# Optimization experiments

Hardware: AMD Instinct MI355X
Metric: run time of the kernel (lower is better)

The kernel has to match this reference:

```python
import jax, jax.numpy as jnp
import numpy as np

B, S, D = 4, 2048, 1024
E = 16          # num_experts
K = 2           # num_experts_per_tok
F = 512         # moe_intermediate_size
FS = 2048       # shared_expert_intermediate_size


def setup_inputs() -> dict:
    key = jax.random.key(0)
    ks = jax.random.split(key, 9)
    s = 0.02
    return {
        "hidden_states": jax.random.normal(ks[0], (B, S, D), jnp.float32),
        "router_w": jax.random.normal(ks[1], (E, D), jnp.float32) * s,   # torch Linear-style [out,in]
        "Wg": jax.random.normal(ks[2], (E, D, F), jnp.float32) * s,      # gate_proj per expert
        "Wu": jax.random.normal(ks[3], (E, D, F), jnp.float32) * s,      # up_proj per expert
        "Wd": jax.random.normal(ks[4], (E, F, D), jnp.float32) * s,      # down_proj per expert
        "Sg": jax.random.normal(ks[5], (D, FS), jnp.float32) * s,        # shared expert gate_proj
        "Su": jax.random.normal(ks[6], (D, FS), jnp.float32) * s,        # shared expert up_proj
        "Sd": jax.random.normal(ks[7], (FS, D), jnp.float32) * s,        # shared expert down_proj
        "shared_gate_w": jax.random.normal(ks[8], (D, 1), jnp.float32) * s,
    }


def reference(hidden_states, router_w, Wg, Wu, Wd, Sg, Su, Sd, shared_gate_w):
    b, s, d = hidden_states.shape
    x = hidden_states.reshape(-1, d)                      # [T, D]
    T = x.shape[0]

    # --- router (Qwen3NextTopKRouter): fp32 softmax -> topk -> renorm ---
    logits = jnp.einsum("td,ed->te", x.astype(jnp.float32), router_w.astype(jnp.float32))
    probs = jax.nn.softmax(logits, axis=-1)               # [T, E]
    top_w, top_i = jax.lax.top_k(probs, K)                # [T, K]
    top_w = top_w / jnp.sum(top_w, axis=-1, keepdims=True)  # norm_topk_prob
    top_w = top_w.astype(x.dtype)

    # dense combine weights [T, E]: zero except at selected experts (index_add semantics)
    dense_w = jnp.zeros((T, E), x.dtype).at[jnp.arange(T)[:, None], top_i].add(top_w)

    # --- experts: SwiGLU per expert, scan over the fixed expert axis ---
    def body(acc, params):
        wg, wu, wd, cw = params                            # cw: [T]
        h = jax.nn.silu(x @ wg) * (x @ wu)                 # [T, F]
        return acc + cw[:, None] * (h @ wd), None

    expert_out, _ = jax.lax.scan(body, jnp.zeros_like(x), (Wg, Wu, Wd, dense_w.T))

    # --- shared expert with sigmoid gate ---
    shared = (jax.nn.silu(x @ Sg) * (x @ Su)) @ Sd         # [T, D]
    shared = jax.nn.sigmoid(x @ shared_gate_w) * shared

    out = expert_out + shared
    return out.reshape(b, s, d)
```

## Files before the change

### kernel.cpp

```cpp
#include <hip/hip_runtime.h>

typedef __attribute__((ext_vector_type(8))) short short8;
typedef __attribute__((ext_vector_type(4))) float f32x4;
typedef unsigned short u16;
typedef unsigned int u32;

#define DEVI __device__ __forceinline__

DEVI u16 f2b(float f) {
  u32 u = __float_as_uint(f);
  u32 r = u + 0x7FFFu + ((u >> 16) & 1u);
  return (u16)(r >> 16);
}
DEVI float b2f(u16 h) { return __uint_as_float(((u32)h) << 16); }
DEVI float silu(float g) { return g / (1.f + __expf(-g)); }

constexpr int T_ = 8192, D_ = 1024, E_ = 16, F_ = 512, FS_ = 2048;

constexpr size_t OFF_XB   = 0;
constexpr size_t OFF_WGU  = OFF_XB  + (size_t)T_ * D_ * 2;
constexpr size_t OFF_WDT  = OFF_WGU + (size_t)E_ * 2 * F_ * D_ * 2;
constexpr size_t OFF_SGU  = OFF_WDT + (size_t)E_ * D_ * F_ * 2;
constexpr size_t OFF_SDT  = OFF_SGU + (size_t)2 * FS_ * D_ * 2;
constexpr size_t OFF_HB   = OFF_SDT + (size_t)D_ * FS_ * 2;
constexpr size_t OFF_HS   = OFF_HB  + (size_t)2 * T_ * F_ * 2;
constexpr size_t OFF_PAIR = OFF_HS  + (size_t)T_ * FS_ * 2;
constexpr size_t OFF_PW   = OFF_PAIR + (size_t)2 * T_ * D_ * 2;
constexpr size_t OFF_GATE = OFF_PW  + (size_t)2 * T_ * 4;
constexpr size_t OFF_CNT  = OFF_GATE + (size_t)T_ * 4;
constexpr size_t OFF_TOP2 = OFF_CNT + 64;
constexpr size_t OFF_LIST = OFF_TOP2 + (size_t)T_ * 4;

__global__ void prep_kernel(
    const float4* __restrict__ x4, const float4* __restrict__ rw4,
    const float4* __restrict__ sgw4, int* __restrict__ top2e,
    float* __restrict__ pw, float* __restrict__ gate, ushort4* __restrict__ xb4,
    const float* __restrict__ Wg, const float* __restrict__ Wu, const float* __restrict__ Wd,
    const float* __restrict__ Sg, const float* __restrict__ Su, const float* __restrict__ Sd,
    u16* __restrict__ wgu, u16* __restrict__ wdT,
    u16* __restrict__ sgu, u16* __restrict__ sdT) {
  const int tid = threadIdx.x;
  const int bid = blockIdx.x;
  if (bid >= 7680) {
    const int lane = tid & 63, wid = tid >> 6;
    const int t = (bid - 7680) * 4 + wid;
    const float4* xr = x4 + (size_t)t * (D_ / 4);
    float acc[17];
#pragma unroll
    for (int e = 0; e < 17; ++e) acc[e] = 0.f;
    ushort4 xo[4];
#pragma unroll
    for (int j = 0; j < 4; ++j) {
      const int d4 = j * 64 + lane;
      float4 xv = xr[d4];
      xo[j] = make_ushort4(f2b(xv.x), f2b(xv.y), f2b(xv.z), f2b(xv.w));
#pragma unroll
      for (int e = 0; e < 16; ++e) {
        float4 wv = rw4[e * 256 + d4];
        acc[e] = fmaf(xv.x, wv.x, fmaf(xv.y, wv.y, fmaf(xv.z, wv.z, fmaf(xv.w, wv.w, acc[e]))));
      }
      float4 sv = sgw4[d4];
      acc[16] = fmaf(xv.x, sv.x, fmaf(xv.y, sv.y, fmaf(xv.z, sv.z, fmaf(xv.w, sv.w, acc[16]))));
    }
#pragma unroll
    for (int j = 0; j < 4; ++j)
      xb4[(size_t)t * 256 + j * 64 + lane] = xo[j];
#pragma unroll
    for (int e = 0; e < 17; ++e) {
      float v = acc[e];
#pragma unroll
      for (int off = 32; off; off >>= 1) v += __shfl_xor(v, off);
      acc[e] = v;
    }
    if (lane == 0) {
      int i1 = 0; float l1 = acc[0];
#pragma unroll
      for (int e = 1; e < 16; ++e) if (acc[e] > l1) { l1 = acc[e]; i1 = e; }
      int i2 = (i1 == 0) ? 1 : 0; float l2 = acc[i2];
#pragma unroll
      for (int e = 0; e < 16; ++e) {
        if (e == i1) continue;
        if (acc[e] > l2) { l2 = acc[e]; i2 = e; }
      }
      float w1 = 1.f / (1.f + expf(l2 - l1));
      top2e[t] = i1 | (i2 << 8);
      pw[2 * t] = w1;
      pw[2 * t + 1] = 1.f - w1;
      gate[t] = 1.f / (1.f + expf(-acc[16]));
    }
    return;
  }
  __shared__ float lds[64][65];
  int i = bid;
  const float* in; u16* out; int R, C, mode, rem;
  if (i < 6144) {
    int j = i >> 11; rem = i & 2047;
    int b = rem >> 7; rem &= 127;
    if (j == 0)      { in = Wg + (size_t)b * D_ * F_; out = wgu + (size_t)b * 2 * F_ * D_; R = D_; C = F_;  mode = 0; }
    else if (j == 1) { in = Wu + (size_t)b * D_ * F_; out = wgu + (size_t)b * 2 * F_ * D_; R = D_; C = F_;  mode = 1; }
    else             { in = Wd + (size_t)b * F_ * D_; out = wdT + (size_t)b * D_ * F_;     R = F_; C = D_;  mode = 2; }
  } else {
    int r2 = i - 6144; int j = r2 >> 9; rem = r2 & 511;
    if (j == 0)      { in = Sg; out = sgu; R = D_;  C = FS_; mode = 0; }
    else if (j == 1) { in = Su; out = sgu; R = D_;  C = FS_; mode = 1; }
    else             { in = Sd; out = sdT; R = FS_; C = D_;  mode = 2; }
  }
  const int ntx = C >> 6;
  const int cx = rem % ntx, cy = rem / ntx;
  const int c0 = cx * 64, r0 = cy * 64;
  {
    const int tx4 = (tid & 15) * 4, ty = tid >> 4;
#pragma unroll
    for (int p = 0; p < 4; ++p) {
      const int rr = ty + p * 16;
      float4 v = *(const float4*)&in[(size_t)(r0 + rr) * C + c0 + tx4];
      lds[rr][tx4] = v.x; lds[rr][tx4 + 1] = v.y; lds[rr][tx4 + 2] = v.z; lds[rr][tx4 + 3] = v.w;
    }
  }
  __syncthreads();
  {
    const int ol = tid >> 2, seg = tid & 3;
    const int f = c0 + ol;
    size_t orow;
    if (mode == 2) orow = f;
    else orow = (size_t)((f >> 4) << 5) + (f & 15) + (mode == 1 ? 16 : 0);
    u16 vals[16];
#pragma unroll
    for (int k = 0; k < 16; ++k) vals[k] = f2b(lds[seg * 16 + k][ol]);
    u16* dst = out + orow * R + r0 + seg * 16;
    *(short8*)dst = *(short8*)&vals[0];
    *(short8*)(dst + 8) = *(short8*)&vals[8];
  }
}

__global__ __launch_bounds__(256) void compact_kernel(
    const int* __restrict__ top2e, int* __restrict__ lists, int* __restrict__ counts) {
  const int e = blockIdx.x;
  const int tid = threadIdx.x, lane = tid & 63, wid = tid >> 6;
  __shared__ int wsum[4];
  __shared__ int base;
  if (tid == 0) base = 0;
  __syncthreads();
  for (int c0 = 0; c0 < T_; c0 += 256) {
    const int t = c0 + tid;
    const int pk = top2e[t];
    int slot = -1;
    if ((pk & 0xFF) == e) slot = 2 * t;
    else if (((pk >> 8) & 0xFF) == e) slot = 2 * t + 1;
    const unsigned long long m = __ballot(slot >= 0);
    const int myofs = __popcll(m & ((1ULL << lane) - 1ULL));
    if (lane == 0) wsum[wid] = __popcll(m);
    __syncthreads();
    const int b = base;
    int wbase = 0;
#pragma unroll
    for (int w = 0; w < 4; ++w) if (w < wid) wbase += wsum[w];
    if (slot >= 0) lists[e * T_ + b + wbase + myofs] = slot;
    __syncthreads();
    if (tid == 0) base += wsum[0] + wsum[1] + wsum[2] + wsum[3];
    __syncthreads();
  }
  if (tid == 0) counts[e] = base;
}

DEVI void gl_lds16(const void* gsrc, void* lds) {
  __builtin_amdgcn_global_load_lds((const __attribute__((address_space(1))) unsigned int*)gsrc,
                                   (__attribute__((address_space(3))) unsigned int*)lds, 16, 0, 0);
}

DEVI void prefix16(const int* counts, int e, int& cnt, int& roff) {
  cnt = counts[e];
  int s = 0;
#pragma unroll
  for (int k = 0; k < E_; ++k) s += (k < e) ? counts[k] : 0;
  roff = s;
}

__global__ __launch_bounds__(256, 2) void gu_gemm(
    const u16* __restrict__ xb, const u16* __restrict__ wgu, const u16* __restrict__ sgu,
    u16* __restrict__ hb, u16* __restrict__ hs,
    const int* __restrict__ counts, const int* __restrict__ lists) {
  extern __shared__ char smem[];
  const int tid = threadIdx.x;
  const int bid = blockIdx.x;
  const bool se = (bid >= 2048);
  int mt, nt, e = 0, cnt = 0, roff = 0;
  const u16* B0;
  if (!se) {
    e = bid >> 7; int r = bid & 127; mt = r >> 3; nt = r & 7;
    prefix16(counts, e, cnt, roff);
    if (mt * 128 >= cnt) return;
    B0 = wgu + (size_t)e * 2 * F_ * D_;
  } else {
    int st = bid - 2048;
    mt = st & 63; nt = st >> 6;
    B0 = sgu;
  }

  const int lane = tid & 63, wid = tid >> 6;
  const int wm = wid >> 1, wn = wid & 1;
  const int lr = lane & 15, lg = lane >> 4;
  const int ldsrow = tid >> 3;
  const int kslot = (tid & 7) << 4;
  constexpr size_t strideB = (size_t)D_ * 2;
  const char* aSrc[4]; const char* bSrc[4];
#pragma unroll
  for (int q = 0; q < 4; ++q) {
    int row = q * 32 + ldsrow;
    int kb = kslot ^ ((row & 7) << 4);
    int r = mt * 128 + row;
    long arow;
    if (!se) arow = (r < cnt) ? (lists[e * T_ + r] >> 1) : 0;
    else arow = r;
    aSrc[q] = (const char*)xb + (size_t)arow * strideB + kb;
    int nrow = nt * 128 + row;
    bSrc[q] = (const char*)B0 + (size_t)nrow * strideB + kb;
  }

  const f32x4 fz = {0.f, 0.f, 0.f, 0.f};
  f32x4 acc[4][4];
#pragma unroll
  for (int i = 0; i < 4; ++i)
#pragma unroll
    for (int j = 0; j < 4; ++j) acc[i][j] = fz;

  const int sw = (lr & 7) << 4;
  constexpr int nks = D_ / 64;

  {
    char* dst = smem;
#pragma unroll
    for (int q = 0; q < 4; ++q) gl_lds16(aSrc[q], dst + q * 4096 + tid * 16);
#pragma unroll
    for (int q = 0; q < 4; ++q) gl_lds16(bSrc[q], dst + 16384 + q * 4096 + tid * 16);
  }
  __syncthreads();

  int cur = 0;
  for (int ks = 0; ks < nks; ++ks) {
    if (ks + 1 < nks) {
      const int kbo = (ks + 1) * 128;
      char* dst = smem + (cur ^ 1) * 32768;
#pragma unroll
      for (int q = 0; q < 4; ++q) gl_lds16(aSrc[q] + kbo, dst + q * 4096 + tid * 16);
#pragma unroll
      for (int q = 0; q < 4; ++q) gl_lds16(bSrc[q] + kbo, dst + 16384 + q * 4096 + tid * 16);
    }
    const char* As = smem + cur * 32768;
    const char* Bs = As + 16384;
#pragma unroll
    for (int kk = 0; kk < 2; ++kk) {
      const int ko = kk * 64 + lg * 16;
      short8 af[4];
#pragma unroll
      for (int fm = 0; fm < 4; ++fm) {
        int row = wm * 64 + fm * 16 + lr;
        af[fm] = *(const short8*)(As + row * 128 + (ko ^ sw));
      }
#pragma unroll
      for (int fn = 0; fn < 4; ++fn) {
        int col = wn * 64 + fn * 16 + lr;
        short8 bf = *(const short8*)(Bs + col * 128 + (ko ^ sw));
#pragma unroll
        for (int fm = 0; fm < 4; ++fm)
          acc[fm][fn] = __builtin_amdgcn_mfma_f32_16x16x32_bf16(af[fm], bf, acc[fm][fn], 0, 0, 0);
      }
    }
    __syncthreads();
    cur ^= 1;
  }

  const int c0 = 16 * (4 * nt + 2 * wn);
  const int r0 = mt * 128;
#pragma unroll
  for (int fm = 0; fm < 4; ++fm) {
#pragma unroll
    for (int j = 0; j < 4; ++j) {
      const int r = r0 + wm * 64 + fm * 16 + lg * 4 + j;
      if (!se && r >= cnt) continue;
      float h0 = silu(acc[fm][0][j]) * acc[fm][1][j];
      float h1 = silu(acc[fm][2][j]) * acc[fm][3][j];
      if (!se) {
        hb[(size_t)(roff + r) * F_ + c0 + lr] = f2b(h0);
        hb[(size_t)(roff + r) * F_ + c0 + 16 + lr] = f2b(h1);
      } else {
        hs[(size_t)r * FS_ + c0 + lr] = f2b(h0);
        hs[(size_t)r * FS_ + c0 + 16 + lr] = f2b(h1);
      }
    }
  }
}

template <int MODE>
__global__ __launch_bounds__(256, 2) void moe_gemm(
    const u16* __restrict__ Abase, const u16* __restrict__ B0,
    u16* __restrict__ outb, float* __restrict__ outf,
    const int* __restrict__ counts, const int* __restrict__ lists,
    const float* __restrict__ pw, const float* __restrict__ gate,
    const u16* __restrict__ pairb, int Kdim) {
  extern __shared__ char smem[];
  const int tid = threadIdx.x;
  const int mt = blockIdx.x, nt = blockIdx.y, e = blockIdx.z;

  int cnt = 0;
  const u16* A = Abase;
  if constexpr (MODE == 1) {
    int roff;
    prefix16(counts, e, cnt, roff);
    if (mt * 128 >= cnt) return;
    A = Abase + (size_t)roff * Kdim;
    B0 += (size_t)e * D_ * F_;
  }

  const int lane = tid & 63, wid = tid >> 6;
  const int wm = wid >> 1, wn = wid & 1;
  const int lr = lane & 15, lg = lane >> 4;
  const int ldsrow = tid >> 3;
  const int kslot = (tid & 7) << 4;
  const size_t strideB = (size_t)Kdim * 2;
  const char* aSrc[4]; const char* bSrc[4];
#pragma unroll
  for (int q = 0; q < 4; ++q) {
    int row = q * 32 + ldsrow;
    int kb = kslot ^ ((row & 7) << 4);
    long arow;
    if constexpr (MODE == 1) {
      int r = mt * 128 + row;
      arow = (r < cnt) ? r : (cnt - 1);
    } else {
      arow = mt * 128 + row;
    }
    aSrc[q] = (const char*)A + (size_t)arow * strideB + kb;
    int nrow = nt * 128 + row;
    bSrc[q] = (const char*)B0 + (size_t)nrow * strideB + kb;
  }

  const f32x4 fz = {0.f, 0.f, 0.f, 0.f};
  f32x4 acc[4][4];
#pragma unroll
  for (int i = 0; i < 4; ++i)
#pragma unroll
    for (int j = 0; j < 4; ++j) acc[i][j] = fz;

  const int nks = Kdim >> 6;
  const int sw = (lr & 7) << 4;

  {
    char* dst = smem;
#pragma unroll
    for (int q = 0; q < 4; ++q) gl_lds16(aSrc[q], dst + q * 4096 + tid * 16);
#pragma unroll
    for (int q = 0; q < 4; ++q) gl_lds16(bSrc[q], dst + 16384 + q * 4096 + tid * 16);
  }
  __syncthreads();

  int cur = 0;
  for (int ks = 0; ks < nks; ++ks) {
    if (ks + 1 < nks) {
      const int kbo = (ks + 1) * 128;
      char* dst = smem + (cur ^ 1) * 32768;
#pragma unroll
      for (int q = 0; q < 4; ++q) gl_lds16(aSrc[q] + kbo, dst + q * 4096 + tid * 16);
#pragma unroll
      for (int q = 0; q < 4; ++q) gl_lds16(bSrc[q] + kbo, dst + 16384 + q * 4096 + tid * 16);
    }
    const char* As = smem + cur * 32768;
    const char* Bs = As + 16384;
#pragma unroll
    for (int kk = 0; kk < 2; ++kk) {
      const int ko = kk * 64 + lg * 16;
      short8 af[4];
#pragma unroll
      for (int fm = 0; fm < 4; ++fm) {
        int row = wm * 64 + fm * 16 + lr;
        af[fm] = *(const short8*)(As + row * 128 + (ko ^ sw));
      }
#pragma unroll
      for (int fn = 0; fn < 4; ++fn) {
        int col = wn * 64 + fn * 16 + lr;
        short8 bf = *(const short8*)(Bs + col * 128 + (ko ^ sw));
#pragma unroll
        for (int fm = 0; fm < 4; ++fm)
          acc[fm][fn] = __builtin_amdgcn_mfma_f32_16x16x32_bf16(af[fm], bf, acc[fm][fn], 0, 0, 0);
      }
    }
    __syncthreads();
    cur ^= 1;
  }

  const int r0 = mt * 128;
#pragma unroll
  for (int fm = 0; fm < 4; ++fm) {
#pragma unroll
    for (int j = 0; j < 4; ++j) {
      const int rowt = wm * 64 + fm * 16 + lg * 4 + j;
      const int r = r0 + rowt;
      if constexpr (MODE == 1) {
        if (r >= cnt) continue;
      }
      int slot = 0;
      float rsc = 0.f;
      if constexpr (MODE == 1) { slot = lists[e * T_ + r]; rsc = pw[slot]; }
      if constexpr (MODE == 3) rsc = gate[r];
#pragma unroll
      for (int fn = 0; fn < 4; ++fn) {
        const int c = nt * 128 + wn * 64 + fn * 16 + lr;
        float v = acc[fm][fn][j];
        if constexpr (MODE == 1) {
          outb[(size_t)slot * D_ + c] = f2b(rsc * v);
        } else {
          float o = v * rsc + b2f(pairb[(size_t)(2 * r) * D_ + c]) + b2f(pairb[(size_t)(2 * r + 1) * D_ + c]);
          outf[(size_t)r * D_ + c] = o;
        }
      }
    }
  }
}

extern "C" void kernel_launch(void* const* d_in, const int* in_sizes, int n_in,
                              void* d_out, int out_size, void* d_ws, size_t ws_size,
                              hipStream_t stream) {
  const float* x   = (const float*)d_in[0];
  const float* rw  = (const float*)d_in[1];
  const float* Wg  = (const float*)d_in[2];
  const float* Wu  = (const float*)d_in[3];
  const float* Wd  = (const float*)d_in[4];
  const float* Sg  = (const float*)d_in[5];
  const float* Su  = (const float*)d_in[6];
  const float* Sd  = (const float*)d_in[7];
  const float* sgw = (const float*)d_in[8];
  float* out = (float*)d_out;

  unsigned char* ws = (unsigned char*)d_ws;
  u16* xb    = (u16*)(ws + OFF_XB);
  u16* wgu   = (u16*)(ws + OFF_WGU);
  u16* wdT   = (u16*)(ws + OFF_WDT);
  u16* sgu   = (u16*)(ws + OFF_SGU);
  u16* sdT   = (u16*)(ws + OFF_SDT);
  u16* hb    = (u16*)(ws + OFF_HB);
  u16* hs    = (u16*)(ws + OFF_HS);
  u16* pairb = (u16*)(ws + OFF_PAIR);
  float* pwf   = (float*)(ws + OFF_PW);
  float* gatef = (float*)(ws + OFF_GATE);
  int* cnti    = (int*)(ws + OFF_CNT);
  int* top2i   = (int*)(ws + OFF_TOP2);
  int* listsi  = (int*)(ws + OFF_LIST);

  prep_kernel<<<9728, 256, 0, stream>>>(
      (const float4*)x, (const float4*)rw, (const float4*)sgw,
      top2i, pwf, gatef, (ushort4*)xb,
      Wg, Wu, Wd, Sg, Su, Sd, wgu, wdT, sgu, sdT);
  compact_kernel<<<E_, 256, 0, stream>>>(top2i, listsi, cnti);

  gu_gemm<<<4096, 256, 65536, stream>>>(xb, wgu, sgu, hb, hs, cnti, listsi);
  moe_gemm<1><<<dim3(16, 8, 16), 256, 65536, stream>>>(hb, wdT, pairb, nullptr,
                                                       cnti, listsi, pwf, gatef, nullptr, 512);
  moe_gemm<3><<<dim3(64, 8, 1), 256, 65536, stream>>>(hs, sdT, nullptr, out,
                                                      cnti, listsi, pwf, gatef, pairb, 2048);

  (void)in_sizes; (void)n_in; (void)out_size; (void)ws_size;
}
```

Baseline: 302.6 us.

## Split K-step into half-stages with fine-grained vmcnt waits and new LDS layout

```diff
diff --git a/kernel.cpp b/kernel.cpp
--- a/kernel.cpp
+++ b/kernel.cpp
@@ -14,6 +14,10 @@
 }
 DEVI float b2f(u16 h) { return __uint_as_float(((u32)h) << 16); }
 DEVI float silu(float g) { return g / (1.f + __expf(-g)); }
+
+DEVI void vm8() { asm volatile("s_waitcnt vmcnt(8)" ::: "memory"); }
+DEVI void vm4() { asm volatile("s_waitcnt vmcnt(4)" ::: "memory"); }
+DEVI void vm0() { asm volatile("s_waitcnt vmcnt(0)" ::: "memory"); }
 
 constexpr int T_ = 8192, D_ = 1024, E_ = 16, F_ = 512, FS_ = 2048;
 
@@ -176,6 +180,52 @@
   roff = s;
 }
 
+#define COMPUTE_KK(base, kk)                                                      \
+  {                                                                               \
+    const char* As_ = (base);                                                     \
+    const char* Bs_ = (base) + 16384;                                             \
+    short8 af[4];                                                                 \
+    _Pragma("unroll")                                                             \
+    for (int fm = 0; fm < 4; ++fm)                                                \
+      af[fm] = *(const short8*)(As_ + (kk) * 8192 + (wm * 64 + fm * 16 + lr) * 64 + rsw); \
+    _Pragma("unroll")                                                             \
+    for (int fn = 0; fn < 4; ++fn) {                                              \
+      short8 bf = *(const short8*)(Bs_ + (kk) * 8192 + (wn * 64 + fn * 16 + lr) * 64 + rsw); \
+      _Pragma("unroll")                                                           \
+      for (int fm = 0; fm < 4; ++fm)                                              \
+        acc[fm][fn] = __builtin_amdgcn_mfma_f32_16x16x32_bf16(af[fm], bf, acc[fm][fn], 0, 0, 0); \
+    }                                                                             \
+  }
+
+#define STAGE_H0(d, o)                                        \
+  { gl_lds16(aR0 + (o), (d) + tid * 16);                      \
+    gl_lds16(aR1 + (o), (d) + 4096 + tid * 16);               \
+    gl_lds16(bR0 + (o), (d) + 16384 + tid * 16);              \
+    gl_lds16(bR1 + (o), (d) + 16384 + 4096 + tid * 16); }
+#define STAGE_H1(d, o)                                        \
+  { gl_lds16(aR0 + (o) + 64, (d) + 8192 + tid * 16);          \
+    gl_lds16(aR1 + (o) + 64, (d) + 8192 + 4096 + tid * 16);   \
+    gl_lds16(bR0 + (o) + 64, (d) + 24576 + tid * 16);         \
+    gl_lds16(bR1 + (o) + 64, (d) + 24576 + 4096 + tid * 16); }
+
+#define KLOOP(NKS)                                            \
+  STAGE_H0(smem, 0); STAGE_H1(smem, 0);                       \
+  int c_ = 0;                                                 \
+  for (int ks = 0; ks < (NKS); ++ks) {                        \
+    const bool pre = (ks + 1 < (NKS));                        \
+    const int o = (ks + 1) * 128;                             \
+    char* d = smem + (c_ ^ 1) * 32768;                        \
+    if (pre) STAGE_H0(d, o);                                  \
+    if (pre) vm8(); else vm4();                               \
+    __builtin_amdgcn_s_barrier();                             \
+    COMPUTE_KK(smem + c_ * 32768, 0);                         \
+    if (pre) STAGE_H1(d, o);                                  \
+    if (pre) vm8(); else vm0();                               \
+    __builtin_amdgcn_s_barrier();                             \
+    COMPUTE_KK(smem + c_ * 32768, 1);                         \
+    c_ ^= 1;                                                  \
+  }
+
 __global__ __launch_bounds__(256, 2) void gu_gemm(
     const u16* __restrict__ xb, const u16* __restrict__ wgu, const u16* __restrict__ sgu,
     u16* __restrict__ hb, u16* __restrict__ hs,
@@ -200,22 +250,23 @@
   const int lane = tid & 63, wid = tid >> 6;
   const int wm = wid >> 1, wn = wid & 1;
   const int lr = lane & 15, lg = lane >> 4;
-  const int ldsrow = tid >> 3;
-  const int kslot = (tid & 7) << 4;
+  const int rsw = (lg ^ ((lr >> 1) & 3)) << 4;
+
+  const int sq = tid >> 2;
+  const int scol = ((tid & 3) ^ ((tid >> 3) & 3)) << 4;
   constexpr size_t strideB = (size_t)D_ * 2;
-  const char* aSrc[4]; const char* bSrc[4];
-#pragma unroll
-  for (int q = 0; q < 4; ++q) {
-    int row = q * 32 + ldsrow;
-    int kb = kslot ^ ((row & 7) << 4);
-    int r = mt * 128 + row;
-    long arow;
-    if (!se) arow = (r < cnt) ? (lists[e * T_ + r] >> 1) : 0;
-    else arow = r;
-    aSrc[q] = (const char*)xb + (size_t)arow * strideB + kb;
-    int nrow = nt * 128 + row;
-    bSrc[q] = (const char*)B0 + (size_t)nrow * strideB + kb;
-  }
+  long ar0, ar1;
+  if (!se) {
+    int r0i = mt * 128 + sq, r1i = mt * 128 + 64 + sq;
+    ar0 = (r0i < cnt) ? (lists[e * T_ + r0i] >> 1) : 0;
+    ar1 = (r1i < cnt) ? (lists[e * T_ + r1i] >> 1) : 0;
+  } else {
+    ar0 = mt * 128 + sq; ar1 = mt * 128 + 64 + sq;
+  }
+  const char* aR0 = (const char*)xb + (size_t)ar0 * strideB + scol;
+  const char* aR1 = (const char*)xb + (size_t)ar1 * strideB + scol;
+  const char* bR0 = (const char*)B0 + (size_t)(nt * 128 + sq) * strideB + scol;
+  const char* bR1 = (const char*)B0 + (size_t)(nt * 128 + 64 + sq) * strideB + scol;
 
   const f32x4 fz = {0.f, 0.f, 0.f, 0.f};
   f32x4 acc[4][4];
@@ -224,51 +275,7 @@
 #pragma unroll
     for (int j = 0; j < 4; ++j) acc[i][j] = fz;
 
-  const int sw = (lr & 7) << 4;
-  constexpr int nks = D_ / 64;
-
-  {
-    char* dst = smem;
-#pragma unroll
-    for (int q = 0; q < 4; ++q) gl_lds16(aSrc[q], dst + q * 4096 + tid * 16);
-#pragma unroll
-    for (int q = 0; q < 4; ++q) gl_lds16(bSrc[q], dst + 16384 + q * 4096 + tid * 16);
-  }
-  __syncthreads();
-
-  int cur = 0;
-  for (int ks = 0; ks < nks; ++ks) {
-    if (ks + 1 < nks) {
-      const int kbo = (ks + 1) * 128;
-      char* dst = smem + (cur ^ 1) * 32768;
-#pragma unroll
-      for (int q = 0; q < 4; ++q) gl_lds16(aSrc[q] + kbo, dst + q * 4096 + tid * 16);
-#pragma unroll
-      for (int q = 0; q < 4; ++q) gl_lds16(bSrc[q] + kbo, dst + 16384 + q * 4096 + tid * 16);
-    }
-    const char* As = smem + cur * 32768;
-    const char* Bs = As + 16384;
-#pragma unroll
-    for (int kk = 0; kk < 2; ++kk) {
-      const int ko = kk * 64 + lg * 16;
-      short8 af[4];
-#pragma unroll
-      for (int fm = 0; fm < 4; ++fm) {
-        int row = wm * 64 + fm * 16 + lr;
-        af[fm] = *(const short8*)(As + row * 128 + (ko ^ sw));
-      }
-#pragma unroll
-      for (int fn = 0; fn < 4; ++fn) {
-        int col = wn * 64 + fn * 16 + lr;
-        short8 bf = *(const short8*)(Bs + col * 128 + (ko ^ sw));
-#pragma unroll
-        for (int fm = 0; fm < 4; ++fm)
-          acc[fm][fn] = __builtin_amdgcn_mfma_f32_16x16x32_bf16(af[fm], bf, acc[fm][fn], 0, 0, 0);
-      }
-    }
-    __syncthreads();
-    cur ^= 1;
-  }
+  KLOOP(16);
 
   const int c0 = 16 * (4 * nt + 2 * wn);
   const int r0 = mt * 128;
@@ -315,25 +322,23 @@
   const int lane = tid & 63, wid = tid >> 6;
   const int wm = wid >> 1, wn = wid & 1;
   const int lr = lane & 15, lg = lane >> 4;
-  const int ldsrow = tid >> 3;
-  const int kslot = (tid & 7) << 4;
+  const int rsw = (lg ^ ((lr >> 1) & 3)) << 4;
+
+  const int sq = tid >> 2;
+  const int scol = ((tid & 3) ^ ((tid >> 3) & 3)) << 4;
   const size_t strideB = (size_t)Kdim * 2;
-  const char* aSrc[4]; const char* bSrc[4];
-#pragma unroll
-  for (int q = 0; q < 4; ++q) {
-    int row = q * 32 + ldsrow;
-    int kb = kslot ^ ((row & 7) << 4);
-    long arow;
-    if constexpr (MODE == 1) {
-      int r = mt * 128 + row;
-      arow = (r < cnt) ? r : (cnt - 1);
-    } else {
-      arow = mt * 128 + row;
-    }
-    aSrc[q] = (const char*)A + (size_t)arow * strideB + kb;
-    int nrow = nt * 128 + row;
-    bSrc[q] = (const char*)B0 + (size_t)nrow * strideB + kb;
-  }
+  long ar0, ar1;
+  if constexpr (MODE == 1) {
+    int r0i = mt * 128 + sq, r1i = mt * 128 + 64 + sq;
+    ar0 = (r0i < cnt) ? r0i : (cnt - 1);
+    ar1 = (r1i < cnt) ? r1i : (cnt - 1);
+  } else {
+    ar0 = mt * 128 + sq; ar1 = mt * 128 + 64 + sq;
+  }
+  const char* aR0 = (const char*)A + (size_t)ar0 * strideB + scol;
+  const char* aR1 = (const char*)A + (size_t)ar1 * strideB + scol;
+  const char* bR0 = (const char*)B0 + (size_t)(nt * 128 + sq) * strideB + scol;
+  const char* bR1 = (const char*)B0 + (size_t)(nt * 128 + 64 + sq) * strideB + scol;
 
   const f32x4 fz = {0.f, 0.f, 0.f, 0.f};
   f32x4 acc[4][4];
@@ -343,50 +348,7 @@
     for (int j = 0; j < 4; ++j) acc[i][j] = fz;
 
   const int nks = Kdim >> 6;
-  const int sw = (lr & 7) << 4;
-
-  {
-    char* dst = smem;
-#pragma unroll
-    for (int q = 0; q < 4; ++q) gl_lds16(aSrc[q], dst + q * 4096 + tid * 16);
-#pragma unroll
-    for (int q = 0; q < 4; ++q) gl_lds16(bSrc[q], dst + 16384 + q * 4096 + tid * 16);
-  }
-  __syncthreads();
-
-  int cur = 0;
-  for (int ks = 0; ks < nks; ++ks) {
-    if (ks + 1 < nks) {
-      const int kbo = (ks + 1) * 128;
-      char* dst = smem + (cur ^ 1) * 32768;
-#pragma unroll
-      for (int q = 0; q < 4; ++q) gl_lds16(aSrc[q] + kbo, dst + q * 4096 + tid * 16);
-#pragma unroll
-      for (int q = 0; q < 4; ++q) gl_lds16(bSrc[q] + kbo, dst + 16384 + q * 4096 + tid * 16);
-    }
-    const char* As = smem + cur * 32768;
-    const char* Bs = As + 16384;
-#pragma unroll
-    for (int kk = 0; kk < 2; ++kk) {
-      const int ko = kk * 64 + lg * 16;
-      short8 af[4];
-#pragma unroll
-      for (int fm = 0; fm < 4; ++fm) {
-        int row = wm * 64 + fm * 16 + lr;
-        af[fm] = *(const short8*)(As + row * 128 + (ko ^ sw));
-      }
-#pragma unroll
-      for (int fn = 0; fn < 4; ++fn) {
-        int col = wn * 64 + fn * 16 + lr;
-        short8 bf = *(const short8*)(Bs + col * 128 + (ko ^ sw));
-#pragma unroll
-        for (int fm = 0; fm < 4; ++fm)
-          acc[fm][fn] = __builtin_amdgcn_mfma_f32_16x16x32_bf16(af[fm], bf, acc[fm][fn], 0, 0, 0);
-      }
-    }
-    __syncthreads();
-    cur ^= 1;
-  }
+  KLOOP(nks);
 
   const int r0 = mt * 128;
 #pragma unroll
```

Result: slower. 317.6 us (+4.9%).
